# Optimization experiments

Measured on AMD Instinct MI355X. Metric: run time of the kernel, lower is better.

Reference implementation:

```python
import jax, jax.numpy as jnp
import numpy as np

B, D, F, FH = 8, 16, 16, 128
L = D * D
EPS = 1e-5


def _coords():
    i = np.arange(L, dtype=np.float64)
    c0 = ((i + 1) / D - D / 2) / (D / 2)
    c1 = ((i + 1) % D - D / 2) / (D / 2)
    return jnp.asarray(np.stack([c0, c1], axis=1), dtype=jnp.float32)  # (L, 2)


def setup_inputs() -> dict:
    key = jax.random.key(0)
    ks = jax.random.split(key, 16)
    s = 0.05
    fin = F + 2
    inp = {
        "x": jax.random.normal(ks[0], (B, F, D, D), jnp.float32),
        # g_fc1 weight split into the x_i half (first f+2 cols) and x_j half
        "W1a": jax.random.normal(ks[1], (fin, FH), jnp.float32) * s,
        "W1b": jax.random.normal(ks[2], (fin, FH), jnp.float32) * s,
        "b1": jnp.zeros((FH,), jnp.float32),
        "g1_gamma": jnp.ones((FH,), jnp.float32), "g1_beta": jnp.zeros((FH,), jnp.float32),
        "W2": jax.random.normal(ks[3], (FH, FH), jnp.float32) * s, "b2": jnp.zeros((FH,), jnp.float32),
        "g2_gamma": jnp.ones((FH,), jnp.float32), "g2_beta": jnp.zeros((FH,), jnp.float32),
        "W3": jax.random.normal(ks[4], (FH, FH), jnp.float32) * s, "b3": jnp.zeros((FH,), jnp.float32),
        "g3_gamma": jnp.ones((FH,), jnp.float32), "g3_beta": jnp.zeros((FH,), jnp.float32),
        "Wagg": jax.random.normal(ks[5], (L,), jnp.float32) * s, "bagg": jnp.zeros((), jnp.float32),
        "Wf": jax.random.normal(ks[6], (FH, FH), jnp.float32) * s, "bf": jnp.zeros((FH,), jnp.float32),
        "f_gamma": jnp.ones((FH,), jnp.float32), "f_beta": jnp.zeros((FH,), jnp.float32),
        "Wo2": jax.random.normal(ks[7], (FH, FH), jnp.float32) * s, "bo2": jnp.zeros((FH,), jnp.float32),
        "o2_gamma": jnp.ones((FH,), jnp.float32), "o2_beta": jnp.zeros((FH,), jnp.float32),
        "Wo3": jax.random.normal(ks[8], (FH, F), jnp.float32) * s, "bo3": jnp.zeros((F,), jnp.float32),
        "coord": _coords(),
    }
    return inp


def _bn(h, gamma, beta):
    # torch BatchNorm1d (training mode) applied over channel dim = last axis here;
    # stats over (batch, length), biased variance.
    mu = jnp.mean(h, axis=(0, 1))
    var = jnp.mean((h - mu) ** 2, axis=(0, 1))
    return gamma * (h - mu) * jax.lax.rsqrt(var + EPS) + beta


def reference(x, W1a, W1b, b1, g1_gamma, g1_beta, W2, b2, g2_gamma, g2_beta,
              W3, b3, g3_gamma, g3_beta, Wagg, bagg, Wf, bf, f_gamma, f_beta,
              Wo2, bo2, o2_gamma, o2_beta, Wo3, bo3, coord):
    b, f, d = x.shape[0], x.shape[1], x.shape[2]
    l = d * d
    x_flat = x.reshape(b, f, l).transpose(0, 2, 1)                     # (b, L, f)
    x_flat = jnp.concatenate([x_flat, jnp.broadcast_to(coord, (b, l, 2))], axis=2)  # (b, L, f+2)
    # g_fc1 on cat([x_i, x_j]): x_i varies along pair-dim2 (index l), x_j along dim1 (index k)
    hi = x_flat @ W1a                                                  # (b, L, FH)
    hj = x_flat @ W1b                                                  # (b, L, FH)
    h = hi[:, None, :, :] + hj[:, :, None, :] + b1                     # (b, L, L, FH)
    h = h.reshape(b, l * l, -1)
    h = jax.nn.relu(_bn(h, g1_gamma, g1_beta))
    h = jax.nn.relu(_bn(h @ W2 + b2, g2_gamma, g2_beta))
    h = jax.nn.relu(_bn(h @ W3 + b3, g3_gamma, g3_beta))
    x_g = h.reshape(b, l, l, -1)                                       # (b, k, l, FH)
    # affine_aggregate: Linear(L -> 1) over the l (dim2) axis after permute
    x_agg = jnp.einsum('bklf,l->bkf', x_g, Wagg) + bagg                # (b, L, FH)
    x_f = jax.nn.relu(_bn(x_agg @ Wf + bf, f_gamma, f_beta))
    xo = jax.nn.relu(_bn(x_f @ Wo2 + bo2, o2_gamma, o2_beta))
    out = xo @ Wo3 + bo3                                               # (b, L, f)
    return out.reshape(b, d, d, f).transpose(0, 3, 1, 2)               # (b, f, d, d)
```

## Files before the change

kernel.cpp:

```cpp
#include <hip/hip_runtime.h>
#include <hip/hip_bf16.h>

typedef __bf16 bf16x8 __attribute__((ext_vector_type(8)));
typedef float  f32x4  __attribute__((ext_vector_type(4)));

static constexpr size_t HI_OFF  = 0;
static constexpr size_t HJ_OFF  = HI_OFF + (1u << 20);
static constexpr size_t Z_OFF   = HJ_OFF + (1u << 20);
static constexpr size_t PS_OFF  = Z_OFF + (size_t)524288 * 128 * 2;
static constexpr size_t PQ_OFF  = PS_OFF + (size_t)4096 * 128 * 4;
static constexpr size_t S1I_OFF = PQ_OFF + (size_t)4096 * 128 * 4;
static constexpr size_t S2I_OFF = S1I_OFF + 4096;
static constexpr size_t S1J_OFF = S2I_OFF + 4096;
static constexpr size_t S2J_OFF = S1J_OFF + 4096;
static constexpr size_t A1_OFF  = S2J_OFF + 4096;
static constexpr size_t D1_OFF  = A1_OFF + 512;
static constexpr size_t A2_OFF  = D1_OFF + 512;
static constexpr size_t C2_OFF  = A2_OFF + 512;
static constexpr size_t A3_OFF  = C2_OFF + 512;
static constexpr size_t C3_OFF  = A3_OFF + 512;
static constexpr size_t AF_OFF  = C3_OFF + 512;
static constexpr size_t CF_OFF  = AF_OFF + 512;
static constexpr size_t AO_OFF  = CF_OFF + 512;
static constexpr size_t CO_OFF  = AO_OFF + 512;
static constexpr size_t W2T_OFF = CO_OFF + 512;
static constexpr size_t W3T_OFF = W2T_OFF + 32768;
static constexpr size_t XAGG_OFF = W3T_OFF + 32768;
static constexpr size_t Y1_OFF  = XAGG_OFF + (1u << 20);
static constexpr size_t Y2_OFF  = Y1_OFF + (1u << 20);
static constexpr size_t TPS_OFF = Y2_OFF + (1u << 20);
static constexpr size_t TPQ_OFF = TPS_OFF + 65536;

__global__ void build_h(const float* __restrict__ x, const float* __restrict__ coord,
                        const float* __restrict__ W1a, const float* __restrict__ W1b,
                        float* __restrict__ hi, float* __restrict__ hj)
{
    __shared__ float xr[18];
    int bl = blockIdx.x;
    int b = bl >> 8, l = bl & 255;
    int t = threadIdx.x;
    if (t < 18)
        xr[t] = (t < 16) ? x[((size_t)b * 16 + t) * 256 + l] : coord[l * 2 + (t - 16)];
    __syncthreads();
    float ai = 0.f, aj = 0.f;
#pragma unroll
    for (int c = 0; c < 18; ++c) {
        float xv = xr[c];
        ai += xv * W1a[c * 128 + t];
        aj += xv * W1b[c * 128 + t];
    }
    hi[(size_t)bl * 128 + t] = ai;
    hj[(size_t)bl * 128 + t] = aj;
}

__global__ void stats1(const float* __restrict__ hi, const float* __restrict__ hj,
                       float* __restrict__ S1i, float* __restrict__ S2i,
                       float* __restrict__ S1j, float* __restrict__ S2j)
{
    int b = blockIdx.x, f = threadIdx.x;
    float s1i = 0, s2i = 0, s1j = 0, s2j = 0;
    for (int l = 0; l < 256; ++l) {
        float vi = hi[((size_t)b * 256 + l) * 128 + f];
        float vj = hj[((size_t)b * 256 + l) * 128 + f];
        s1i += vi; s2i += vi * vi;
        s1j += vj; s2j += vj * vj;
    }
    S1i[b * 128 + f] = s1i; S2i[b * 128 + f] = s2i;
    S1j[b * 128 + f] = s1j; S2j[b * 128 + f] = s2j;
}

__global__ void bn1_finalize(const float* __restrict__ S1i, const float* __restrict__ S2i,
                             const float* __restrict__ S1j, const float* __restrict__ S2j,
                             const float* __restrict__ g, const float* __restrict__ be,
                             float* __restrict__ a1, float* __restrict__ d1,
                             const float* __restrict__ W2, const float* __restrict__ W3,
                             __bf16* __restrict__ W2t, __bf16* __restrict__ W3t)
{
    int f = threadIdx.x;
    float s1i = 0, s2i = 0, s1j = 0, s2j = 0;
    float mib[8], mjb[8];
#pragma unroll
    for (int b = 0; b < 8; ++b) {
        float x1 = S1i[b * 128 + f]; s1i += x1; mib[b] = x1 * (1.f / 256.f);
        s2i += S2i[b * 128 + f];
        float x2 = S1j[b * 128 + f]; s1j += x2; mjb[b] = x2 * (1.f / 256.f);
        s2j += S2j[b * 128 + f];
    }
    const float invN = 1.f / 2048.f;
    float mi = s1i * invN, mj = s1j * invN;
    float vu = s2i * invN - mi * mi;
    float vv = s2j * invN - mj * mj;
    float cr = 0.f;
#pragma unroll
    for (int b = 0; b < 8; ++b) cr += (mib[b] - mi) * (mjb[b] - mj);
    cr *= (1.f / 8.f);
    float var = vu + vv + 2.f * cr;
    float av = g[f] * rsqrtf(var + 1e-5f);
    a1[f] = av;
    d1[f] = be[f] - av * (mi + mj);
    for (int k = 0; k < 128; ++k) {
        W2t[f * 128 + k] = (__bf16)W2[k * 128 + f];
        W3t[f * 128 + k] = (__bf16)W3[k * 128 + f];
    }
}

__global__ __launch_bounds__(256) void pair_gemm1(
    const float* __restrict__ hi, const float* __restrict__ hj,
    const float* __restrict__ a1, const float* __restrict__ d1,
    const __bf16* __restrict__ W2t,
    __bf16* __restrict__ Z, float* __restrict__ ps, float* __restrict__ pq)
{
    __shared__ __align__(16) char hA[32768];
    __shared__ __align__(16) char wB[32768];
    __shared__ float red[1024];

    int blk = blockIdx.x;
    int half = blk & 1;
    int bk = blk >> 1;
    int b = bk >> 8;
    int t = threadIdx.x;
    int lane = t & 63;
    int wave = t >> 6;
    int fc = (t & 15) * 8;
    int rg = t >> 4;

    float a1v[8], qv[8];
    const float* hjrow = hj + (size_t)bk * 128 + fc;
    const float* d1p = d1 + fc;
    const float* a1p = a1 + fc;
#pragma unroll
    for (int j = 0; j < 8; ++j) { a1v[j] = a1p[j]; qv[j] = a1v[j] * hjrow[j] + d1p[j]; }

    const float* hib = hi + ((size_t)b * 256 + half * 128) * 128;
#pragma unroll
    for (int rr = 0; rr < 128; rr += 16) {
        int row = rr + rg;
        const float* src = hib + row * 128 + fc;
        bf16x8 v;
#pragma unroll
        for (int j = 0; j < 8; ++j) {
            float h = fmaxf(a1v[j] * src[j] + qv[j], 0.f);
            v[j] = (__bf16)h;
        }
        int byte = (row * 256 + fc * 2) ^ ((row & 7) << 4);
        *reinterpret_cast<bf16x8*>(hA + byte) = v;
        bf16x8 w = *reinterpret_cast<const bf16x8*>(W2t + row * 128 + fc);
        *reinterpret_cast<bf16x8*>(wB + byte) = w;
    }
    __syncthreads();

    f32x4 acc[2][8] = {};
    int arow0 = wave * 32 + (lane & 15);
    int kg = (lane >> 4) * 8;
#pragma unroll
    for (int kk = 0; kk < 128; kk += 32) {
        bf16x8 af[2], bfr[8];
#pragma unroll
        for (int m = 0; m < 2; ++m) {
            int row = arow0 + m * 16;
            int byte = (row * 256 + (kk + kg) * 2) ^ ((row & 7) << 4);
            af[m] = *reinterpret_cast<const bf16x8*>(hA + byte);
        }
#pragma unroll
        for (int n = 0; n < 8; ++n) {
            int col = n * 16 + (lane & 15);
            int byte = (col * 256 + (kk + kg) * 2) ^ ((col & 7) << 4);
            bfr[n] = *reinterpret_cast<const bf16x8*>(wB + byte);
        }
#pragma unroll
        for (int m = 0; m < 2; ++m)
#pragma unroll
            for (int n = 0; n < 8; ++n)
                acc[m][n] = __builtin_amdgcn_mfma_f32_16x16x32_bf16(af[m], bfr[n], acc[m][n], 0, 0, 0);
    }

    __bf16* zb = Z + ((size_t)bk * 256 + half * 128) * 128;
    float s[8] = {}, q[8] = {};
    int r0 = (lane >> 4) * 4;
    int cl = lane & 15;
#pragma unroll
    for (int m = 0; m < 2; ++m)
#pragma unroll
        for (int n = 0; n < 8; ++n)
#pragma unroll
            for (int r = 0; r < 4; ++r) {
                float v = acc[m][n][r];
                int row = wave * 32 + m * 16 + r0 + r;
                zb[row * 128 + n * 16 + cl] = (__bf16)v;
                s[n] += v; q[n] += v * v;
            }
#pragma unroll
    for (int n = 0; n < 8; ++n) {
        s[n] += __shfl_xor(s[n], 16); s[n] += __shfl_xor(s[n], 32);
        q[n] += __shfl_xor(q[n], 16); q[n] += __shfl_xor(q[n], 32);
    }
    if (lane < 16) {
#pragma unroll
        for (int n = 0; n < 8; ++n) {
            red[wave * 256 + n * 16 + cl] = s[n];
            red[wave * 256 + 128 + n * 16 + cl] = q[n];
        }
    }
    __syncthreads();
    {
        int f = t & 127, which = t >> 7;
        float a = red[0 * 256 + which * 128 + f] + red[1 * 256 + which * 128 + f]
                + red[2 * 256 + which * 128 + f] + red[3 * 256 + which * 128 + f];
        if (which == 0) ps[(size_t)blk * 128 + f] = a;
        else            pq[(size_t)blk * 128 + f] = a;
    }
}

__global__ __launch_bounds__(256) void pair_gemm2(
    __bf16* __restrict__ Z,
    const float* __restrict__ a2, const float* __restrict__ c2,
    const __bf16* __restrict__ W3t,
    float* __restrict__ ps, float* __restrict__ pq)
{
    __shared__ __align__(16) char hA[32768];
    __shared__ __align__(16) char wB[32768];
    __shared__ float red[1024];

    int blk = blockIdx.x;
    int half = blk & 1;
    int bk = blk >> 1;
    int t = threadIdx.x;
    int lane = t & 63;
    int wave = t >> 6;
    int fc = (t & 15) * 8;
    int rg = t >> 4;

    float a2v[8], c2v[8];
#pragma unroll
    for (int j = 0; j < 8; ++j) { a2v[j] = a2[fc + j]; c2v[j] = c2[fc + j]; }

    __bf16* zbase = Z + ((size_t)bk * 256 + half * 128) * 128;
#pragma unroll
    for (int rr = 0; rr < 128; rr += 16) {
        int row = rr + rg;
        bf16x8 zv = *reinterpret_cast<const bf16x8*>(zbase + row * 128 + fc);
        bf16x8 v;
#pragma unroll
        for (int j = 0; j < 8; ++j) {
            float h = fmaxf(a2v[j] * (float)zv[j] + c2v[j], 0.f);
            v[j] = (__bf16)h;
        }
        int byte = (row * 256 + fc * 2) ^ ((row & 7) << 4);
        *reinterpret_cast<bf16x8*>(hA + byte) = v;
        bf16x8 w = *reinterpret_cast<const bf16x8*>(W3t + row * 128 + fc);
        *reinterpret_cast<bf16x8*>(wB + byte) = w;
    }
    __syncthreads();

    f32x4 acc[2][8] = {};
    int arow0 = wave * 32 + (lane & 15);
    int kg = (lane >> 4) * 8;
#pragma unroll
    for (int kk = 0; kk < 128; kk += 32) {
        bf16x8 af[2], bfr[8];
#pragma unroll
        for (int m = 0; m < 2; ++m) {
            int row = arow0 + m * 16;
            int byte = (row * 256 + (kk + kg) * 2) ^ ((row & 7) << 4);
            af[m] = *reinterpret_cast<const bf16x8*>(hA + byte);
        }
#pragma unroll
        for (int n = 0; n < 8; ++n) {
            int col = n * 16 + (lane & 15);
            int byte = (col * 256 + (kk + kg) * 2) ^ ((col & 7) << 4);
            bfr[n] = *reinterpret_cast<const bf16x8*>(wB + byte);
        }
#pragma unroll
        for (int m = 0; m < 2; ++m)
#pragma unroll
            for (int n = 0; n < 8; ++n)
                acc[m][n] = __builtin_amdgcn_mfma_f32_16x16x32_bf16(af[m], bfr[n], acc[m][n], 0, 0, 0);
    }

    float s[8] = {}, q[8] = {};
    int r0 = (lane >> 4) * 4;
    int cl = lane & 15;
#pragma unroll
    for (int m = 0; m < 2; ++m)
#pragma unroll
        for (int n = 0; n < 8; ++n)
#pragma unroll
            for (int r = 0; r < 4; ++r) {
                float v = acc[m][n][r];
                int row = wave * 32 + m * 16 + r0 + r;
                zbase[row * 128 + n * 16 + cl] = (__bf16)v;
                s[n] += v; q[n] += v * v;
            }
#pragma unroll
    for (int n = 0; n < 8; ++n) {
        s[n] += __shfl_xor(s[n], 16); s[n] += __shfl_xor(s[n], 32);
        q[n] += __shfl_xor(q[n], 16); q[n] += __shfl_xor(q[n], 32);
    }
    if (lane < 16) {
#pragma unroll
        for (int n = 0; n < 8; ++n) {
            red[wave * 256 + n * 16 + cl] = s[n];
            red[wave * 256 + 128 + n * 16 + cl] = q[n];
        }
    }
    __syncthreads();
    {
        int f = t & 127, which = t >> 7;
        float a = red[0 * 256 + which * 128 + f] + red[1 * 256 + which * 128 + f]
                + red[2 * 256 + which * 128 + f] + red[3 * 256 + which * 128 + f];
        if (which == 0) ps[(size_t)blk * 128 + f] = a;
        else            pq[(size_t)blk * 128 + f] = a;
    }
}

__global__ void finalize_bn(const float* __restrict__ ps, const float* __restrict__ pq,
                            int nblk, float inv_count,
                            const float* __restrict__ gamma, const float* __restrict__ beta,
                            float* __restrict__ a, float* __restrict__ c)
{
    __shared__ float rs[256], rq[256];
    int f = blockIdx.x, t = threadIdx.x;
    float s = 0, q = 0;
    for (int i = t; i < nblk; i += 256) {
        s += ps[(size_t)i * 128 + f];
        q += pq[(size_t)i * 128 + f];
    }
    rs[t] = s; rq[t] = q;
    __syncthreads();
    for (int st = 128; st > 0; st >>= 1) {
        if (t < st) { rs[t] += rs[t + st]; rq[t] += rq[t + st]; }
        __syncthreads();
    }
    if (t == 0) {
        float mean = rs[0] * inv_count;
        float var = rq[0] * inv_count - mean * mean;
        float av = gamma[f] * rsqrtf(var + 1e-5f);
        a[f] = av;
        c[f] = beta[f] - av * mean;
    }
}

__global__ void aggregate(const __bf16* __restrict__ Z,
                          const float* __restrict__ a3, const float* __restrict__ c3,
                          const float* __restrict__ Wagg, const float* __restrict__ bagg,
                          float* __restrict__ xagg)
{
    int bk = blockIdx.x;
    int f = threadIdx.x;
    const __bf16* zb = Z + (size_t)bk * 256 * 128 + f;
    float av = a3[f], cv = c3[f];
    float acc = 0.f;
#pragma unroll 4
    for (int l = 0; l < 256; ++l) {
        float v = (float)zb[(size_t)l * 128];
        v = fmaxf(av * v + cv, 0.f);
        acc += v * Wagg[l];
    }
    xagg[(size_t)bk * 128 + f] = acc + bagg[0];
}

__global__ void tail_gemm(const float* __restrict__ X,
                          const float* __restrict__ aIn, const float* __restrict__ cIn, int relu_in,
                          const float* __restrict__ W, const float* __restrict__ bias,
                          float* __restrict__ Y, float* __restrict__ ps, float* __restrict__ pq)
{
    __shared__ float xs[2048];
    __shared__ float rsum[256];
    int blk = blockIdx.x, t = threadIdx.x;
    for (int i = t; i < 2048; i += 256) {
        float v = X[(size_t)blk * 2048 + i];
        if (relu_in) { int f = i & 127; v = fmaxf(aIn[f] * v + cIn[f], 0.f); }
        xs[i] = v;
    }
    __syncthreads();
    int col = t & 127, hf = t >> 7;
    float bv = bias[col];
    float acc[8];
#pragma unroll
    for (int r = 0; r < 8; ++r) acc[r] = bv;
    for (int k = 0; k < 128; ++k) {
        float w = W[k * 128 + col];
#pragma unroll
        for (int r = 0; r < 8; ++r) acc[r] += xs[(hf * 8 + r) * 128 + k] * w;
    }
    float s = 0, q = 0;
#pragma unroll
    for (int r = 0; r < 8; ++r) {
        Y[((size_t)blk * 16 + hf * 8 + r) * 128 + col] = acc[r];
        s += acc[r]; q += acc[r] * acc[r];
    }
    rsum[t] = s; __syncthreads();
    if (hf == 0) ps[(size_t)blk * 128 + col] = rsum[col] + rsum[128 + col];
    __syncthreads();
    rsum[t] = q; __syncthreads();
    if (hf == 0) pq[(size_t)blk * 128 + col] = rsum[col] + rsum[128 + col];
}

__global__ void tail_out(const float* __restrict__ Y2,
                         const float* __restrict__ ao, const float* __restrict__ co,
                         const float* __restrict__ Wo3, const float* __restrict__ bo3,
                         float* __restrict__ out)
{
    __shared__ float xs[2048];
    int blk = blockIdx.x, t = threadIdx.x;
    for (int i = t; i < 2048; i += 256) {
        int f = i & 127;
        xs[i] = fmaxf(ao[f] * Y2[(size_t)blk * 2048 + i] + co[f], 0.f);
    }
    __syncthreads();
    int col = t & 15, r = t >> 4;
    float acc = bo3[col];
    for (int k = 0; k < 128; ++k) acc += xs[r * 128 + k] * Wo3[k * 16 + col];
    int grow = blk * 16 + r;
    int b = grow >> 8, l = grow & 255;
    out[((size_t)b * 16 + col) * 256 + l] = acc;
}

extern "C" void kernel_launch(void* const* d_in, const int* in_sizes, int n_in,
                              void* d_out, int out_size, void* d_ws, size_t ws_size,
                              hipStream_t stream)
{
    const float* x     = (const float*)d_in[0];
    const float* W1a   = (const float*)d_in[1];
    const float* W1b   = (const float*)d_in[2];
    const float* g1g   = (const float*)d_in[4];
    const float* g1b   = (const float*)d_in[5];
    const float* W2    = (const float*)d_in[6];
    const float* g2g   = (const float*)d_in[8];
    const float* g2b   = (const float*)d_in[9];
    const float* W3    = (const float*)d_in[10];
    const float* g3g   = (const float*)d_in[12];
    const float* g3b   = (const float*)d_in[13];
    const float* Wagg  = (const float*)d_in[14];
    const float* bagg  = (const float*)d_in[15];
    const float* Wf    = (const float*)d_in[16];
    const float* bf_   = (const float*)d_in[17];
    const float* fg    = (const float*)d_in[18];
    const float* fb    = (const float*)d_in[19];
    const float* Wo2   = (const float*)d_in[20];
    const float* bo2   = (const float*)d_in[21];
    const float* og    = (const float*)d_in[22];
    const float* ob    = (const float*)d_in[23];
    const float* Wo3   = (const float*)d_in[24];
    const float* bo3   = (const float*)d_in[25];
    const float* coord = (const float*)d_in[26];

    char* ws = (char*)d_ws;
    float*  HI   = (float*)(ws + HI_OFF);
    float*  HJ   = (float*)(ws + HJ_OFF);
    __bf16* Z    = (__bf16*)(ws + Z_OFF);
    float*  PS   = (float*)(ws + PS_OFF);
    float*  PQ   = (float*)(ws + PQ_OFF);
    float*  S1I  = (float*)(ws + S1I_OFF);
    float*  S2I  = (float*)(ws + S2I_OFF);
    float*  S1J  = (float*)(ws + S1J_OFF);
    float*  S2J  = (float*)(ws + S2J_OFF);
    float*  A1   = (float*)(ws + A1_OFF);
    float*  D1   = (float*)(ws + D1_OFF);
    float*  A2   = (float*)(ws + A2_OFF);
    float*  C2   = (float*)(ws + C2_OFF);
    float*  A3   = (float*)(ws + A3_OFF);
    float*  C3   = (float*)(ws + C3_OFF);
    float*  AF   = (float*)(ws + AF_OFF);
    float*  CF   = (float*)(ws + CF_OFF);
    float*  AO   = (float*)(ws + AO_OFF);
    float*  CO   = (float*)(ws + CO_OFF);
    __bf16* W2T  = (__bf16*)(ws + W2T_OFF);
    __bf16* W3T  = (__bf16*)(ws + W3T_OFF);
    float*  XAGG = (float*)(ws + XAGG_OFF);
    float*  Y1   = (float*)(ws + Y1_OFF);
    float*  Y2   = (float*)(ws + Y2_OFF);
    float*  TPS  = (float*)(ws + TPS_OFF);
    float*  TPQ  = (float*)(ws + TPQ_OFF);

    build_h<<<2048, 128, 0, stream>>>(x, coord, W1a, W1b, HI, HJ);
    stats1<<<8, 128, 0, stream>>>(HI, HJ, S1I, S2I, S1J, S2J);
    bn1_finalize<<<1, 128, 0, stream>>>(S1I, S2I, S1J, S2J, g1g, g1b, A1, D1, W2, W3, W2T, W3T);

    pair_gemm1<<<4096, 256, 0, stream>>>(HI, HJ, A1, D1, W2T, Z, PS, PQ);
    finalize_bn<<<128, 256, 0, stream>>>(PS, PQ, 4096, 1.f / 524288.f, g2g, g2b, A2, C2);

    pair_gemm2<<<4096, 256, 0, stream>>>(Z, A2, C2, W3T, PS, PQ);
    finalize_bn<<<128, 256, 0, stream>>>(PS, PQ, 4096, 1.f / 524288.f, g3g, g3b, A3, C3);

    aggregate<<<2048, 128, 0, stream>>>(Z, A3, C3, Wagg, bagg, XAGG);

    tail_gemm<<<128, 256, 0, stream>>>(XAGG, A1, D1, 0, Wf, bf_, Y1, TPS, TPQ);
    finalize_bn<<<128, 256, 0, stream>>>(TPS, TPQ, 128, 1.f / 2048.f, fg, fb, AF, CF);

    tail_gemm<<<128, 256, 0, stream>>>(Y1, AF, CF, 1, Wo2, bo2, Y2, TPS, TPQ);
    finalize_bn<<<128, 256, 0, stream>>>(TPS, TPQ, 128, 1.f / 2048.f, og, ob, AO, CO);

    tail_out<<<128, 256, 0, stream>>>(Y2, AO, CO, Wo3, bo3, (float*)d_out);

    (void)in_sizes; (void)n_in; (void)out_size; (void)ws_size;
}
```

Measured before the change: 217.1 us.

## Parallelize stats and weight transpose, read GEMM weights from global, vectorize aggregate

stats1 is split across 64 blocks instead of 8, and bn1_finalize sums the partial results. The serial 128-iteration weight transpose moves out of the single-block bn1_finalize into its own 128-block kernel. The pair GEMMs no longer stage W2t/W3t in shared memory and load the B fragments straight from global/L2, which halves LDS use per block and may raise occupancy, at the cost of repeated global loads. aggregate now uses 256 threads with bf16x8 vector loads and a shared-memory reduction over row groups.

```diff
diff --git a/kernel.cpp b/kernel.cpp
--- a/kernel.cpp
+++ b/kernel.cpp
@@ -4,16 +4,17 @@
 typedef __bf16 bf16x8 __attribute__((ext_vector_type(8)));
 typedef float  f32x4  __attribute__((ext_vector_type(4)));
 
+static constexpr size_t MB = 1u << 20;
 static constexpr size_t HI_OFF  = 0;
-static constexpr size_t HJ_OFF  = HI_OFF + (1u << 20);
-static constexpr size_t Z_OFF   = HJ_OFF + (1u << 20);
+static constexpr size_t HJ_OFF  = HI_OFF + MB;
+static constexpr size_t Z_OFF   = HJ_OFF + MB;
 static constexpr size_t PS_OFF  = Z_OFF + (size_t)524288 * 128 * 2;
 static constexpr size_t PQ_OFF  = PS_OFF + (size_t)4096 * 128 * 4;
 static constexpr size_t S1I_OFF = PQ_OFF + (size_t)4096 * 128 * 4;
-static constexpr size_t S2I_OFF = S1I_OFF + 4096;
-static constexpr size_t S1J_OFF = S2I_OFF + 4096;
-static constexpr size_t S2J_OFF = S1J_OFF + 4096;
-static constexpr size_t A1_OFF  = S2J_OFF + 4096;
+static constexpr size_t S2I_OFF = S1I_OFF + 32768;
+static constexpr size_t S1J_OFF = S2I_OFF + 32768;
+static constexpr size_t S2J_OFF = S1J_OFF + 32768;
+static constexpr size_t A1_OFF  = S2J_OFF + 32768;
 static constexpr size_t D1_OFF  = A1_OFF + 512;
 static constexpr size_t A2_OFF  = D1_OFF + 512;
 static constexpr size_t C2_OFF  = A2_OFF + 512;
@@ -26,9 +27,9 @@
 static constexpr size_t W2T_OFF = CO_OFF + 512;
 static constexpr size_t W3T_OFF = W2T_OFF + 32768;
 static constexpr size_t XAGG_OFF = W3T_OFF + 32768;
-static constexpr size_t Y1_OFF  = XAGG_OFF + (1u << 20);
-static constexpr size_t Y2_OFF  = Y1_OFF + (1u << 20);
-static constexpr size_t TPS_OFF = Y2_OFF + (1u << 20);
+static constexpr size_t Y1_OFF  = XAGG_OFF + MB;
+static constexpr size_t Y2_OFF  = Y1_OFF + MB;
+static constexpr size_t TPS_OFF = Y2_OFF + MB;
 static constexpr size_t TPQ_OFF = TPS_OFF + 65536;
 
 __global__ void build_h(const float* __restrict__ x, const float* __restrict__ coord,
@@ -57,34 +58,41 @@
                        float* __restrict__ S1i, float* __restrict__ S2i,
                        float* __restrict__ S1j, float* __restrict__ S2j)
 {
-    int b = blockIdx.x, f = threadIdx.x;
+    int g = blockIdx.x;
+    int b = g >> 3, lg = g & 7;
+    int f = threadIdx.x;
     float s1i = 0, s2i = 0, s1j = 0, s2j = 0;
-    for (int l = 0; l < 256; ++l) {
+#pragma unroll 4
+    for (int i = 0; i < 32; ++i) {
+        int l = lg * 32 + i;
         float vi = hi[((size_t)b * 256 + l) * 128 + f];
         float vj = hj[((size_t)b * 256 + l) * 128 + f];
         s1i += vi; s2i += vi * vi;
         s1j += vj; s2j += vj * vj;
     }
-    S1i[b * 128 + f] = s1i; S2i[b * 128 + f] = s2i;
-    S1j[b * 128 + f] = s1j; S2j[b * 128 + f] = s2j;
+    S1i[g * 128 + f] = s1i; S2i[g * 128 + f] = s2i;
+    S1j[g * 128 + f] = s1j; S2j[g * 128 + f] = s2j;
 }
 
 __global__ void bn1_finalize(const float* __restrict__ S1i, const float* __restrict__ S2i,
                              const float* __restrict__ S1j, const float* __restrict__ S2j,
                              const float* __restrict__ g, const float* __restrict__ be,
-                             float* __restrict__ a1, float* __restrict__ d1,
-                             const float* __restrict__ W2, const float* __restrict__ W3,
-                             __bf16* __restrict__ W2t, __bf16* __restrict__ W3t)
+                             float* __restrict__ a1, float* __restrict__ d1)
 {
     int f = threadIdx.x;
     float s1i = 0, s2i = 0, s1j = 0, s2j = 0;
     float mib[8], mjb[8];
 #pragma unroll
     for (int b = 0; b < 8; ++b) {
-        float x1 = S1i[b * 128 + f]; s1i += x1; mib[b] = x1 * (1.f / 256.f);
-        s2i += S2i[b * 128 + f];
-        float x2 = S1j[b * 128 + f]; s1j += x2; mjb[b] = x2 * (1.f / 256.f);
-        s2j += S2j[b * 128 + f];
+        float sb = 0, sbj = 0;
+#pragma unroll
+        for (int lg = 0; lg < 8; ++lg) {
+            int gg = b * 8 + lg;
+            sb  += S1i[gg * 128 + f]; s2i += S2i[gg * 128 + f];
+            sbj += S1j[gg * 128 + f]; s2j += S2j[gg * 128 + f];
+        }
+        mib[b] = sb * (1.f / 256.f); mjb[b] = sbj * (1.f / 256.f);
+        s1i += sb; s1j += sbj;
     }
     const float invN = 1.f / 2048.f;
     float mi = s1i * invN, mj = s1j * invN;
@@ -98,10 +106,14 @@
     float av = g[f] * rsqrtf(var + 1e-5f);
     a1[f] = av;
     d1[f] = be[f] - av * (mi + mj);
-    for (int k = 0; k < 128; ++k) {
-        W2t[f * 128 + k] = (__bf16)W2[k * 128 + f];
-        W3t[f * 128 + k] = (__bf16)W3[k * 128 + f];
-    }
+}
+
+__global__ void transpose_w(const float* __restrict__ W2, const float* __restrict__ W3,
+                            __bf16* __restrict__ W2t, __bf16* __restrict__ W3t)
+{
+    int f = blockIdx.x, k = threadIdx.x;
+    W2t[f * 128 + k] = (__bf16)W2[k * 128 + f];
+    W3t[f * 128 + k] = (__bf16)W3[k * 128 + f];
 }
 
 __global__ __launch_bounds__(256) void pair_gemm1(
@@ -111,7 +123,6 @@
     __bf16* __restrict__ Z, float* __restrict__ ps, float* __restrict__ pq)
 {
     __shared__ __align__(16) char hA[32768];
-    __shared__ __align__(16) char wB[32768];
     __shared__ float red[1024];
 
     int blk = blockIdx.x;
@@ -144,14 +155,13 @@
         }
         int byte = (row * 256 + fc * 2) ^ ((row & 7) << 4);
         *reinterpret_cast<bf16x8*>(hA + byte) = v;
-        bf16x8 w = *reinterpret_cast<const bf16x8*>(W2t + row * 128 + fc);
-        *reinterpret_cast<bf16x8*>(wB + byte) = w;
     }
     __syncthreads();
 
     f32x4 acc[2][8] = {};
     int arow0 = wave * 32 + (lane & 15);
     int kg = (lane >> 4) * 8;
+    int cl = lane & 15;
 #pragma unroll
     for (int kk = 0; kk < 128; kk += 32) {
         bf16x8 af[2], bfr[8];
@@ -162,11 +172,8 @@
             af[m] = *reinterpret_cast<const bf16x8*>(hA + byte);
         }
 #pragma unroll
-        for (int n = 0; n < 8; ++n) {
-            int col = n * 16 + (lane & 15);
-            int byte = (col * 256 + (kk + kg) * 2) ^ ((col & 7) << 4);
-            bfr[n] = *reinterpret_cast<const bf16x8*>(wB + byte);
-        }
+        for (int n = 0; n < 8; ++n)
+            bfr[n] = *reinterpret_cast<const bf16x8*>(W2t + (n * 16 + cl) * 128 + kk + kg);
 #pragma unroll
         for (int m = 0; m < 2; ++m)
 #pragma unroll
@@ -177,7 +184,6 @@
     __bf16* zb = Z + ((size_t)bk * 256 + half * 128) * 128;
     float s[8] = {}, q[8] = {};
     int r0 = (lane >> 4) * 4;
-    int cl = lane & 15;
 #pragma unroll
     for (int m = 0; m < 2; ++m)
 #pragma unroll
@@ -218,7 +224,6 @@
     float* __restrict__ ps, float* __restrict__ pq)
 {
     __shared__ __align__(16) char hA[32768];
-    __shared__ __align__(16) char wB[32768];
     __shared__ float red[1024];
 
     int blk = blockIdx.x;
@@ -247,14 +252,13 @@
         }
         int byte = (row * 256 + fc * 2) ^ ((row & 7) << 4);
         *reinterpret_cast<bf16x8*>(hA + byte) = v;
-        bf16x8 w = *reinterpret_cast<const bf16x8*>(W3t + row * 128 + fc);
-        *reinterpret_cast<bf16x8*>(wB + byte) = w;
     }
     __syncthreads();
 
     f32x4 acc[2][8] = {};
     int arow0 = wave * 32 + (lane & 15);
     int kg = (lane >> 4) * 8;
+    int cl = lane & 15;
 #pragma unroll
     for (int kk = 0; kk < 128; kk += 32) {
         bf16x8 af[2], bfr[8];
@@ -265,11 +269,8 @@
             af[m] = *reinterpret_cast<const bf16x8*>(hA + byte);
         }
 #pragma unroll
-        for (int n = 0; n < 8; ++n) {
-            int col = n * 16 + (lane & 15);
-            int byte = (col * 256 + (kk + kg) * 2) ^ ((col & 7) << 4);
-            bfr[n] = *reinterpret_cast<const bf16x8*>(wB + byte);
-        }
+        for (int n = 0; n < 8; ++n)
+            bfr[n] = *reinterpret_cast<const bf16x8*>(W3t + (n * 16 + cl) * 128 + kk + kg);
 #pragma unroll
         for (int m = 0; m < 2; ++m)
 #pragma unroll
@@ -279,7 +280,6 @@
 
     float s[8] = {}, q[8] = {};
     int r0 = (lane >> 4) * 4;
-    int cl = lane & 15;
 #pragma unroll
     for (int m = 0; m < 2; ++m)
 #pragma unroll
@@ -340,23 +340,41 @@
     }
 }
 
-__global__ void aggregate(const __bf16* __restrict__ Z,
-                          const float* __restrict__ a3, const float* __restrict__ c3,
-                          const float* __restrict__ Wagg, const float* __restrict__ bagg,
-                          float* __restrict__ xagg)
-{
+__global__ __launch_bounds__(256) void aggregate(
+    const __bf16* __restrict__ Z,
+    const float* __restrict__ a3, const float* __restrict__ c3,
+    const float* __restrict__ Wagg, const float* __restrict__ bagg,
+    float* __restrict__ xagg)
+{
+    __shared__ float red[16 * 128];
     int bk = blockIdx.x;
-    int f = threadIdx.x;
-    const __bf16* zb = Z + (size_t)bk * 256 * 128 + f;
-    float av = a3[f], cv = c3[f];
-    float acc = 0.f;
+    int t = threadIdx.x;
+    int fc = t & 15;
+    int g = t >> 4;
+    float av[8], cv[8];
+#pragma unroll
+    for (int j = 0; j < 8; ++j) { av[j] = a3[fc * 8 + j]; cv[j] = c3[fc * 8 + j]; }
+
+    const __bf16* zb = Z + (size_t)bk * 256 * 128;
+    float acc[8] = {};
 #pragma unroll 4
-    for (int l = 0; l < 256; ++l) {
-        float v = (float)zb[(size_t)l * 128];
-        v = fmaxf(av * v + cv, 0.f);
-        acc += v * Wagg[l];
-    }
-    xagg[(size_t)bk * 128 + f] = acc + bagg[0];
+    for (int i = 0; i < 16; ++i) {
+        int l = g * 16 + i;
+        bf16x8 zv = *reinterpret_cast<const bf16x8*>(zb + (size_t)l * 128 + fc * 8);
+        float w = Wagg[l];
+#pragma unroll
+        for (int j = 0; j < 8; ++j)
+            acc[j] += fmaxf(av[j] * (float)zv[j] + cv[j], 0.f) * w;
+    }
+#pragma unroll
+    for (int j = 0; j < 8; ++j) red[g * 128 + fc * 8 + j] = acc[j];
+    __syncthreads();
+    if (t < 128) {
+        float s = 0;
+#pragma unroll
+        for (int gg = 0; gg < 16; ++gg) s += red[gg * 128 + t];
+        xagg[(size_t)bk * 128 + t] = s + bagg[0];
+    }
 }
 
 __global__ void tail_gemm(const float* __restrict__ X,
@@ -474,8 +492,9 @@
     float*  TPQ  = (float*)(ws + TPQ_OFF);
 
     build_h<<<2048, 128, 0, stream>>>(x, coord, W1a, W1b, HI, HJ);
-    stats1<<<8, 128, 0, stream>>>(HI, HJ, S1I, S2I, S1J, S2J);
-    bn1_finalize<<<1, 128, 0, stream>>>(S1I, S2I, S1J, S2J, g1g, g1b, A1, D1, W2, W3, W2T, W3T);
+    stats1<<<64, 128, 0, stream>>>(HI, HJ, S1I, S2I, S1J, S2J);
+    bn1_finalize<<<1, 128, 0, stream>>>(S1I, S2I, S1J, S2J, g1g, g1b, A1, D1);
+    transpose_w<<<128, 128, 0, stream>>>(W2, W3, W2T, W3T);
 
     pair_gemm1<<<4096, 256, 0, stream>>>(HI, HJ, A1, D1, W2T, Z, PS, PQ);
     finalize_bn<<<128, 256, 0, stream>>>(PS, PQ, 4096, 1.f / 524288.f, g2g, g2b, A2, C2);
@@ -483,7 +502,7 @@
     pair_gemm2<<<4096, 256, 0, stream>>>(Z, A2, C2, W3T, PS, PQ);
     finalize_bn<<<128, 256, 0, stream>>>(PS, PQ, 4096, 1.f / 524288.f, g3g, g3b, A3, C3);
 
-    aggregate<<<2048, 128, 0, stream>>>(Z, A3, C3, Wagg, bagg, XAGG);
+    aggregate<<<2048, 256, 0, stream>>>(Z, A3, C3, Wagg, bagg, XAGG);
 
     tail_gemm<<<128, 256, 0, stream>>>(XAGG, A1, D1, 0, Wf, bf_, Y1, TPS, TPQ);
     finalize_bn<<<128, 256, 0, stream>>>(TPS, TPQ, 128, 1.f / 2048.f, fg, fb, AF, CF);
```

Measured after the change: 278.2 us. 1.28x slower.
